# Kernel optimization log

Hardware: AMD Instinct MI355X
Metric: run time of the kernel (lower is better)

## Reference

```python
import jax, jax.numpy as jnp
import numpy as np

N_MID, EMB_DIM, HID, SEQ_LEN, BATCH = 200000, 128, 128, 256, 512


def setup_inputs() -> dict:
    key = jax.random.key(0)
    k1, k2, k3, k4, k5, k6, k7 = jax.random.split(key, 7)
    mid = jax.random.randint(k1, (BATCH,), 0, N_MID, dtype=jnp.int32)
    mid_hist = jax.random.randint(k2, (BATCH, SEQ_LEN), 0, N_MID, dtype=jnp.int32)
    mask = jax.random.randint(k3, (BATCH, SEQ_LEN), 0, 2, dtype=jnp.int32)
    # Embedding table: RandomUniform(-0.05, 0.05) per original init
    emb_table = jax.random.uniform(k4, (N_MID, EMB_DIM), jnp.float32, -0.05, 0.05)
    # Keras GRU (reset_after=True): kernel [D,3H], recurrent_kernel [H,3H], bias [2,3H]
    W = jax.random.normal(k5, (EMB_DIM, 3 * HID), jnp.float32) * 0.05
    U = jax.random.normal(k6, (HID, 3 * HID), jnp.float32) * 0.05
    b = jax.random.normal(k7, (2, 3 * HID), jnp.float32) * 0.05
    return {"mid": mid, "mid_hist": mid_hist, "mask": mask,
            "emb_table": emb_table, "W": W, "U": U, "b": b}


def _masked_gru(hist_emb, mask, W, U, b):
    # hist_emb: [B, T, D], mask: [B, T] int
    B, T, _ = hist_emb.shape
    H = U.shape[0]
    b_in, b_rec = b[0], b[1]
    # precompute input projections once: [B, T, 3H]
    x_proj = jnp.einsum('btd,dh->bth', hist_emb, W) + b_in
    x_proj_t = jnp.swapaxes(x_proj, 0, 1)  # [T, B, 3H]
    mask_t = jnp.swapaxes(mask, 0, 1).astype(bool)  # [T, B]

    def step(h, inp):
        x_t, m_t = inp
        rec = h @ U + b_rec  # [B, 3H]
        xz, xr, xh = x_t[:, :H], x_t[:, H:2 * H], x_t[:, 2 * H:]
        rz, rr, rh = rec[:, :H], rec[:, H:2 * H], rec[:, 2 * H:]
        z = jax.nn.sigmoid(xz + rz)
        r = jax.nn.sigmoid(xr + rr)
        hh = jnp.tanh(xh + r * rh)  # reset_after=True: r applied after recurrent matmul
        h_new = z * h + (1.0 - z) * hh
        h = jnp.where(m_t[:, None], h_new, h)  # masked steps hold state
        return h, None

    h0 = jnp.zeros((B, H), hist_emb.dtype)
    h_final, _ = jax.lax.scan(step, h0, (x_proj_t, mask_t))
    return h_final


def reference(mid, mid_hist, mask, emb_table, W, U, b):
    item_emb = emb_table[mid]            # [B, D]
    hist_emb = emb_table[mid_hist]       # [B, T, D]
    user_vec = _masked_gru(hist_emb, mask, W, U, b)  # [B, H]
    return (user_vec, item_emb)
```

## Files before the change

kernel.cpp:

```cpp
#include <hip/hip_runtime.h>

#define BATCH  512
#define SEQLEN 256
#define EMB    128
#define HID    128
#define LDSROW 136

typedef _Float16 f16;
typedef __attribute__((ext_vector_type(8))) _Float16 half8;
typedef __attribute__((ext_vector_type(4))) _Float16 half4f;
typedef __attribute__((ext_vector_type(4))) float    floatx4;

__device__ __forceinline__ float fast_sigmoid(float x) {
    return __builtin_amdgcn_rcpf(1.0f + __builtin_amdgcn_exp2f(x * -1.4426950408889634f));
}
__device__ __forceinline__ float fast_tanh(float x) {
    float t = __builtin_amdgcn_exp2f(x * 2.8853900817779268f);
    return 1.0f - 2.0f * __builtin_amdgcn_rcpf(t + 1.0f);
}

__global__ void prep_kernel(const int* __restrict__ mask, const int* __restrict__ mid,
                            const float* __restrict__ emb,
                            unsigned* __restrict__ maskP, float* __restrict__ item_out) {
    int tid  = blockIdx.x * blockDim.x + threadIdx.x;
    int nthr = gridDim.x * blockDim.x;
    for (int i = tid; i < 32 * SEQLEN; i += nthr) {
        int blk = i >> 8, t = i & 255;
        unsigned m = 0;
        #pragma unroll
        for (int r = 0; r < 16; ++r)
            m |= (unsigned)(mask[(blk * 16 + r) * SEQLEN + t] & 1) << r;
        maskP[i] = m;
    }
    for (int i = tid; i < BATCH * EMB; i += nthr) {
        int b = i >> 7, d = i & 127;
        item_out[i] = emb[(size_t)mid[b] * EMB + d];
    }
}

__global__ __launch_bounds__(512, 1) void gru_fused(
        const int* __restrict__ mid_hist, const float* __restrict__ emb,
        const float* __restrict__ W, const float* __restrict__ U,
        const float* __restrict__ bvec, const unsigned* __restrict__ maskP,
        float* __restrict__ out_user) {
    __shared__ __align__(16) f16 elds[2][16 * LDSROW];
    __shared__ __align__(16) f16 hpk[16 * LDSROW];

    const int tid   = threadIdx.x;
    const int lane  = tid & 63;
    const int w     = tid >> 6;
    const int l15   = lane & 15;
    const int g4    = lane >> 4;
    const int blk   = blockIdx.x;
    const int bbase = blk * 16;

    half8 uA[3][4], wA[3][4];
    #pragma unroll
    for (int p = 0; p < 3; ++p)
        #pragma unroll
        for (int kt = 0; kt < 4; ++kt) {
            half8 u, v;
            const int j = p * 128 + w * 16 + l15;
            #pragma unroll
            for (int e = 0; e < 8; ++e) {
                int k = kt * 32 + g4 * 8 + e;
                u[e] = (f16)U[k * 384 + j];
                v[e] = (f16)W[k * 384 + j];
            }
            uA[p][kt] = u; wA[p][kt] = v;
        }

    const int jj = w * 16 + g4 * 4;
    float bcz[4], bcr[4], bih[4], brh[4];
    {
        float4 a0 = *(const float4*)(bvec + jj);
        float4 a1 = *(const float4*)(bvec + 384 + jj);
        float4 c0 = *(const float4*)(bvec + 128 + jj);
        float4 c1 = *(const float4*)(bvec + 512 + jj);
        float4 d0 = *(const float4*)(bvec + 256 + jj);
        float4 d1 = *(const float4*)(bvec + 640 + jj);
        bcz[0]=a0.x+a1.x; bcz[1]=a0.y+a1.y; bcz[2]=a0.z+a1.z; bcz[3]=a0.w+a1.w;
        bcr[0]=c0.x+c1.x; bcr[1]=c0.y+c1.y; bcr[2]=c0.z+c1.z; bcr[3]=c0.w+c1.w;
        bih[0]=d0.x; bih[1]=d0.y; bih[2]=d0.z; bih[3]=d0.w;
        brh[0]=d1.x; brh[1]=d1.y; brh[2]=d1.z; brh[3]=d1.w;
    }

    const int r_e = tid >> 5;
    const int c_e = (tid & 31) * 4;

    for (int i = tid; i < 16 * LDSROW; i += 512) hpk[i] = (f16)0.f;

    {
        int i0 = mid_hist[(bbase + r_e) * SEQLEN + 0];
        int i1 = mid_hist[(bbase + r_e) * SEQLEN + 1];
        float4 v0 = *(const float4*)(emb + (size_t)i0 * EMB + c_e);
        float4 v1 = *(const float4*)(emb + (size_t)i1 * EMB + c_e);
        *(half4f*)&elds[0][r_e * LDSROW + c_e] = half4f{(f16)v0.x,(f16)v0.y,(f16)v0.z,(f16)v0.w};
        *(half4f*)&elds[1][r_e * LDSROW + c_e] = half4f{(f16)v1.x,(f16)v1.y,(f16)v1.z,(f16)v1.w};
    }
    __syncthreads();

    int i2 = mid_hist[(bbase + r_e) * SEQLEN + 2];
    int i3 = mid_hist[(bbase + r_e) * SEQLEN + 3];
    float4   eE   = *(const float4*)(emb + (size_t)i2 * EMB + c_e);
    float4   eO   = *(const float4*)(emb + (size_t)i3 * EMB + c_e);
    int      idxE = mid_hist[(bbase + r_e) * SEQLEN + 4];
    int      idxO = mid_hist[(bbase + r_e) * SEQLEN + 5];
    unsigned mskE = maskP[blk * SEQLEN + 0];
    unsigned mskO = maskP[blk * SEQLEN + 1];

    float hreg[4] = {0.f, 0.f, 0.f, 0.f};
    const int aoff  = l15 * LDSROW;
    const int hwoff = l15 * LDSROW + jj;

    auto step = [&](int t, int slot, float4& eBuf, int& idxP, unsigned& mskR) {
        half8 ea[4], ha[4];
        const f16* eb = elds[slot];
        #pragma unroll
        for (int kt = 0; kt < 4; ++kt) {
            ea[kt] = *(const half8*)&eb [aoff + kt * 32 + g4 * 8];
            ha[kt] = *(const half8*)&hpk[aoff + kt * 32 + g4 * 8];
        }
        __builtin_amdgcn_sched_barrier(0);
        asm volatile("s_waitcnt lgkmcnt(0)" ::: "memory");
        __builtin_amdgcn_s_barrier();
        __builtin_amdgcn_sched_barrier(0);

        float4 ev = eBuf;
        *(half4f*)&elds[slot][r_e * LDSROW + c_e] =
            half4f{(f16)ev.x,(f16)ev.y,(f16)ev.z,(f16)ev.w};
        unsigned mval = mskR;
        int ii = idxP;
        eBuf = *(const float4*)(emb + (size_t)ii * EMB + c_e);
        int t6 = t + 6 < SEQLEN ? t + 6 : SEQLEN - 1;
        idxP = mid_hist[(bbase + r_e) * SEQLEN + t6];
        int t2 = t + 2 < SEQLEN ? t + 2 : SEQLEN - 1;
        mskR = maskP[blk * SEQLEN + t2];

        floatx4 az = {0,0,0,0}, ar = {0,0,0,0}, axh = {0,0,0,0}, arh = {0,0,0,0};
        #pragma unroll
        for (int kt = 0; kt < 4; ++kt) {
            az  = __builtin_amdgcn_mfma_f32_16x16x32_f16(wA[0][kt], ea[kt], az,  0,0,0);
            ar  = __builtin_amdgcn_mfma_f32_16x16x32_f16(wA[1][kt], ea[kt], ar,  0,0,0);
            axh = __builtin_amdgcn_mfma_f32_16x16x32_f16(wA[2][kt], ea[kt], axh, 0,0,0);
            az  = __builtin_amdgcn_mfma_f32_16x16x32_f16(uA[0][kt], ha[kt], az,  0,0,0);
            ar  = __builtin_amdgcn_mfma_f32_16x16x32_f16(uA[1][kt], ha[kt], ar,  0,0,0);
            arh = __builtin_amdgcn_mfma_f32_16x16x32_f16(uA[2][kt], ha[kt], arh, 0,0,0);
        }

        const int mbit = (mval >> l15) & 1;
        #pragma unroll
        for (int r = 0; r < 4; ++r) {
            float z  = fast_sigmoid(az[r] + bcz[r]);
            float rg = fast_sigmoid(ar[r] + bcr[r]);
            float hh = fast_tanh(axh[r] + bih[r] + rg * (arh[r] + brh[r]));
            float hn = hh + z * (hreg[r] - hh);
            hreg[r] = mbit ? hn : hreg[r];
        }
        half4f hw = { (f16)hreg[0], (f16)hreg[1], (f16)hreg[2], (f16)hreg[3] };
        *(half4f*)&hpk[hwoff] = hw;
        __builtin_amdgcn_sched_barrier(0);
        asm volatile("s_waitcnt lgkmcnt(0)" ::: "memory");
        __builtin_amdgcn_s_barrier();
        __builtin_amdgcn_sched_barrier(0);
    };

    #pragma unroll 1
    for (int t = 0; t < SEQLEN; t += 2) {
        step(t,     0, eE, idxE, mskE);
        step(t + 1, 1, eO, idxO, mskO);
    }

    float4 o = { hreg[0], hreg[1], hreg[2], hreg[3] };
    *(float4*)(out_user + (size_t)(bbase + l15) * HID + jj) = o;
}

extern "C" void kernel_launch(void* const* d_in, const int* in_sizes, int n_in,
                              void* d_out, int out_size, void* d_ws, size_t ws_size,
                              hipStream_t stream) {
    const int*   mid      = (const int*)d_in[0];
    const int*   mid_hist = (const int*)d_in[1];
    const int*   mask     = (const int*)d_in[2];
    const float* emb      = (const float*)d_in[3];
    const float* W        = (const float*)d_in[4];
    const float* U        = (const float*)d_in[5];
    const float* bvec     = (const float*)d_in[6];

    float* user_out = (float*)d_out;
    float* item_out = (float*)d_out + BATCH * HID;

    unsigned* maskP = (unsigned*)d_ws;

    prep_kernel<<<32, 256, 0, stream>>>(mask, mid, emb, maskP, item_out);
    gru_fused  <<<32, 512, 0, stream>>>(mid_hist, emb, W, U, bvec, maskP, user_out);
}
```

Before: 398.5 us.

## Double-buffer hidden state and 4-slot embedding ring to halve barriers per step

Makes the hidden-state LDS tile double-buffered and the embedding tile a four-slot ring, so each GRU step needs one barrier instead of two. Embedding operands for the next step are prefetched from LDS during the current step. An XOR swizzle replaces the padded row layout to avoid LDS bank conflicts, and the gate math folds the log2e scales into FMAs. The prep kernel is split into mask-packing blocks that stage through LDS and separate item-gather blocks. Risks include ring-slot hazards, a wrong step ordering around the single barrier, and higher register pressure from holding the prefetched operands.

```diff
diff --git a/kernel.cpp b/kernel.cpp
--- a/kernel.cpp
+++ b/kernel.cpp
@@ -4,47 +4,49 @@
 #define SEQLEN 256
 #define EMB    128
 #define HID    128
-#define LDSROW 136
 
 typedef _Float16 f16;
 typedef __attribute__((ext_vector_type(8))) _Float16 half8;
 typedef __attribute__((ext_vector_type(4))) _Float16 half4f;
 typedef __attribute__((ext_vector_type(4))) float    floatx4;
 
-__device__ __forceinline__ float fast_sigmoid(float x) {
-    return __builtin_amdgcn_rcpf(1.0f + __builtin_amdgcn_exp2f(x * -1.4426950408889634f));
-}
-__device__ __forceinline__ float fast_tanh(float x) {
-    float t = __builtin_amdgcn_exp2f(x * 2.8853900817779268f);
-    return 1.0f - 2.0f * __builtin_amdgcn_rcpf(t + 1.0f);
+#define L2E 1.44269504088896340736f
+#define T2E 2.88539008177792681472f
+
+__device__ __forceinline__ int swzB(int byte) {
+    return byte ^ (((byte >> 8) & 7) << 4);
 }
 
 __global__ void prep_kernel(const int* __restrict__ mask, const int* __restrict__ mid,
                             const float* __restrict__ emb,
                             unsigned* __restrict__ maskP, float* __restrict__ item_out) {
-    int tid  = blockIdx.x * blockDim.x + threadIdx.x;
-    int nthr = gridDim.x * blockDim.x;
-    for (int i = tid; i < 32 * SEQLEN; i += nthr) {
-        int blk = i >> 8, t = i & 255;
+    const int bid = blockIdx.x, tid = threadIdx.x;
+    if (bid < 32) {
+        __shared__ int mls[16 * 256];
+        for (int i = tid; i < 16 * 256; i += 256)
+            mls[i] = mask[bid * 16 * 256 + i];
+        __syncthreads();
+        int t = tid;
         unsigned m = 0;
         #pragma unroll
         for (int r = 0; r < 16; ++r)
-            m |= (unsigned)(mask[(blk * 16 + r) * SEQLEN + t] & 1) << r;
-        maskP[i] = m;
-    }
-    for (int i = tid; i < BATCH * EMB; i += nthr) {
-        int b = i >> 7, d = i & 127;
-        item_out[i] = emb[(size_t)mid[b] * EMB + d];
-    }
-}
-
-__global__ __launch_bounds__(512, 1) void gru_fused(
+            m |= (unsigned)(mls[r * 256 + t] & 1) << r;
+        maskP[bid * 256 + t] = m;
+    } else {
+        for (int i = (bid - 32) * 256 + tid; i < BATCH * EMB; i += 224 * 256) {
+            int b = i >> 7, d = i & 127;
+            item_out[i] = emb[(size_t)mid[b] * EMB + d];
+        }
+    }
+}
+
+__global__ __launch_bounds__(512, 2) void gru_fused(
         const int* __restrict__ mid_hist, const float* __restrict__ emb,
         const float* __restrict__ W, const float* __restrict__ U,
         const float* __restrict__ bvec, const unsigned* __restrict__ maskP,
         float* __restrict__ out_user) {
-    __shared__ __align__(16) f16 elds[2][16 * LDSROW];
-    __shared__ __align__(16) f16 hpk[16 * LDSROW];
+    __shared__ __align__(16) f16 hpk[2][16 * 128];
+    __shared__ __align__(16) f16 elds[4][16 * 128];
 
     const int tid   = threadIdx.x;
     const int lane  = tid & 63;
@@ -71,7 +73,7 @@
         }
 
     const int jj = w * 16 + g4 * 4;
-    float bcz[4], bcr[4], bih[4], brh[4];
+    float nbz[4], nbr[4], sxh[4], srh[4];
     {
         float4 a0 = *(const float4*)(bvec + jj);
         float4 a1 = *(const float4*)(bvec + 384 + jj);
@@ -79,63 +81,57 @@
         float4 c1 = *(const float4*)(bvec + 512 + jj);
         float4 d0 = *(const float4*)(bvec + 256 + jj);
         float4 d1 = *(const float4*)(bvec + 640 + jj);
-        bcz[0]=a0.x+a1.x; bcz[1]=a0.y+a1.y; bcz[2]=a0.z+a1.z; bcz[3]=a0.w+a1.w;
-        bcr[0]=c0.x+c1.x; bcr[1]=c0.y+c1.y; bcr[2]=c0.z+c1.z; bcr[3]=c0.w+c1.w;
-        bih[0]=d0.x; bih[1]=d0.y; bih[2]=d0.z; bih[3]=d0.w;
-        brh[0]=d1.x; brh[1]=d1.y; brh[2]=d1.z; brh[3]=d1.w;
-    }
-
-    const int r_e = tid >> 5;
-    const int c_e = (tid & 31) * 4;
-
-    for (int i = tid; i < 16 * LDSROW; i += 512) hpk[i] = (f16)0.f;
+        nbz[0] = -L2E*(a0.x+a1.x); nbz[1] = -L2E*(a0.y+a1.y);
+        nbz[2] = -L2E*(a0.z+a1.z); nbz[3] = -L2E*(a0.w+a1.w);
+        nbr[0] = -L2E*(c0.x+c1.x); nbr[1] = -L2E*(c0.y+c1.y);
+        nbr[2] = -L2E*(c0.z+c1.z); nbr[3] = -L2E*(c0.w+c1.w);
+        sxh[0] =  T2E*d0.x; sxh[1] = T2E*d0.y; sxh[2] = T2E*d0.z; sxh[3] = T2E*d0.w;
+        srh[0] =  T2E*d1.x; srh[1] = T2E*d1.y; srh[2] = T2E*d1.z; srh[3] = T2E*d1.w;
+    }
+
+    int aswz[4];
+    #pragma unroll
+    for (int kt = 0; kt < 4; ++kt)
+        aswz[kt] = swzB(l15 * 256 + kt * 64 + g4 * 16) >> 1;
+    const int hswz = swzB(l15 * 256 + jj * 2) >> 1;
+    const int r_e  = tid >> 5;
+    const int c32  = tid & 31;
+    const int sswz = swzB(r_e * 256 + c32 * 8) >> 1;
+    const int histbase = (bbase + r_e) * SEQLEN;
+    const int mpbase   = blk * SEQLEN;
+
+    for (int i = tid; i < 16 * 128; i += 512) hpk[0][i] = (f16)0.f;
 
     {
-        int i0 = mid_hist[(bbase + r_e) * SEQLEN + 0];
-        int i1 = mid_hist[(bbase + r_e) * SEQLEN + 1];
-        float4 v0 = *(const float4*)(emb + (size_t)i0 * EMB + c_e);
-        float4 v1 = *(const float4*)(emb + (size_t)i1 * EMB + c_e);
-        *(half4f*)&elds[0][r_e * LDSROW + c_e] = half4f{(f16)v0.x,(f16)v0.y,(f16)v0.z,(f16)v0.w};
-        *(half4f*)&elds[1][r_e * LDSROW + c_e] = half4f{(f16)v1.x,(f16)v1.y,(f16)v1.z,(f16)v1.w};
-    }
+        int i0 = mid_hist[histbase + 0];
+        int i1 = mid_hist[histbase + 1];
+        float4 v0 = *(const float4*)(emb + (size_t)i0 * EMB + c32 * 4);
+        float4 v1 = *(const float4*)(emb + (size_t)i1 * EMB + c32 * 4);
+        *(half4f*)&elds[0][sswz] = half4f{(f16)v0.x,(f16)v0.y,(f16)v0.z,(f16)v0.w};
+        *(half4f*)&elds[1][sswz] = half4f{(f16)v1.x,(f16)v1.y,(f16)v1.z,(f16)v1.w};
+    }
+    int i2 = mid_hist[histbase + 2];
+    int i3 = mid_hist[histbase + 3];
+    float4   Ee = *(const float4*)(emb + (size_t)i2 * EMB + c32 * 4);
+    float4   Eo = *(const float4*)(emb + (size_t)i3 * EMB + c32 * 4);
+    int      Ie = mid_hist[histbase + 4];
+    int      Io = mid_hist[histbase + 5];
+    unsigned Me = maskP[mpbase + 0];
+    unsigned Mo = maskP[mpbase + 1];
+
+    float hreg[4] = {0.f, 0.f, 0.f, 0.f};
     __syncthreads();
 
-    int i2 = mid_hist[(bbase + r_e) * SEQLEN + 2];
-    int i3 = mid_hist[(bbase + r_e) * SEQLEN + 3];
-    float4   eE   = *(const float4*)(emb + (size_t)i2 * EMB + c_e);
-    float4   eO   = *(const float4*)(emb + (size_t)i3 * EMB + c_e);
-    int      idxE = mid_hist[(bbase + r_e) * SEQLEN + 4];
-    int      idxO = mid_hist[(bbase + r_e) * SEQLEN + 5];
-    unsigned mskE = maskP[blk * SEQLEN + 0];
-    unsigned mskO = maskP[blk * SEQLEN + 1];
-
-    float hreg[4] = {0.f, 0.f, 0.f, 0.f};
-    const int aoff  = l15 * LDSROW;
-    const int hwoff = l15 * LDSROW + jj;
-
-    auto step = [&](int t, int slot, float4& eBuf, int& idxP, unsigned& mskR) {
-        half8 ea[4], ha[4];
-        const f16* eb = elds[slot];
-        #pragma unroll
-        for (int kt = 0; kt < 4; ++kt) {
-            ea[kt] = *(const half8*)&eb [aoff + kt * 32 + g4 * 8];
-            ha[kt] = *(const half8*)&hpk[aoff + kt * 32 + g4 * 8];
-        }
-        __builtin_amdgcn_sched_barrier(0);
-        asm volatile("s_waitcnt lgkmcnt(0)" ::: "memory");
-        __builtin_amdgcn_s_barrier();
-        __builtin_amdgcn_sched_barrier(0);
-
-        float4 ev = eBuf;
-        *(half4f*)&elds[slot][r_e * LDSROW + c_e] =
-            half4f{(f16)ev.x,(f16)ev.y,(f16)ev.z,(f16)ev.w};
-        unsigned mval = mskR;
-        int ii = idxP;
-        eBuf = *(const float4*)(emb + (size_t)ii * EMB + c_e);
-        int t6 = t + 6 < SEQLEN ? t + 6 : SEQLEN - 1;
-        idxP = mid_hist[(bbase + r_e) * SEQLEN + t6];
-        int t2 = t + 2 < SEQLEN ? t + 2 : SEQLEN - 1;
-        mskR = maskP[blk * SEQLEN + t2];
+    half8 ea[4];
+    #pragma unroll
+    for (int kt = 0; kt < 4; ++kt) ea[kt] = *(const half8*)&elds[0][aswz[kt]];
+
+    auto step = [&](int t, float4& E, int& I, unsigned& M) {
+        const f16* hrd = hpk[t & 1];
+        f16*       hwr = hpk[(t + 1) & 1];
+        half8 ha[4];
+        #pragma unroll
+        for (int kt = 0; kt < 4; ++kt) ha[kt] = *(const half8*)&hrd[aswz[kt]];
 
         floatx4 az = {0,0,0,0}, ar = {0,0,0,0}, axh = {0,0,0,0}, arh = {0,0,0,0};
         #pragma unroll
@@ -143,22 +139,41 @@
             az  = __builtin_amdgcn_mfma_f32_16x16x32_f16(wA[0][kt], ea[kt], az,  0,0,0);
             ar  = __builtin_amdgcn_mfma_f32_16x16x32_f16(wA[1][kt], ea[kt], ar,  0,0,0);
             axh = __builtin_amdgcn_mfma_f32_16x16x32_f16(wA[2][kt], ea[kt], axh, 0,0,0);
+        }
+        #pragma unroll
+        for (int kt = 0; kt < 4; ++kt) {
             az  = __builtin_amdgcn_mfma_f32_16x16x32_f16(uA[0][kt], ha[kt], az,  0,0,0);
             ar  = __builtin_amdgcn_mfma_f32_16x16x32_f16(uA[1][kt], ha[kt], ar,  0,0,0);
             arh = __builtin_amdgcn_mfma_f32_16x16x32_f16(uA[2][kt], ha[kt], arh, 0,0,0);
         }
 
+        *(half4f*)&elds[(t + 2) & 3][sswz] =
+            half4f{(f16)E.x, (f16)E.y, (f16)E.z, (f16)E.w};
+        int ii = I;
+        E = *(const float4*)(emb + (size_t)ii * EMB + c32 * 4);
+        int t6 = t + 6 < SEQLEN ? t + 6 : SEQLEN - 1;
+        I = mid_hist[histbase + t6];
+        unsigned mval = M;
+        M = maskP[mpbase + t + 2];
+        {
+            const f16* erd = elds[(t + 1) & 3];
+            #pragma unroll
+            for (int kt = 0; kt < 4; ++kt) ea[kt] = *(const half8*)&erd[aswz[kt]];
+        }
+
         const int mbit = (mval >> l15) & 1;
         #pragma unroll
         for (int r = 0; r < 4; ++r) {
-            float z  = fast_sigmoid(az[r] + bcz[r]);
-            float rg = fast_sigmoid(ar[r] + bcr[r]);
-            float hh = fast_tanh(axh[r] + bih[r] + rg * (arh[r] + brh[r]));
-            float hn = hh + z * (hreg[r] - hh);
-            hreg[r] = mbit ? hn : hreg[r];
-        }
-        half4f hw = { (f16)hreg[0], (f16)hreg[1], (f16)hreg[2], (f16)hreg[3] };
-        *(half4f*)&hpk[hwoff] = hw;
+            float z  = __builtin_amdgcn_rcpf(1.f + __builtin_amdgcn_exp2f(__builtin_fmaf(az[r], -L2E, nbz[r])));
+            float rg = __builtin_amdgcn_rcpf(1.f + __builtin_amdgcn_exp2f(__builtin_fmaf(ar[r], -L2E, nbr[r])));
+            float u  = __builtin_fmaf(rg, __builtin_fmaf(arh[r], T2E, srh[r]),
+                                          __builtin_fmaf(axh[r], T2E, sxh[r]));
+            float hh = __builtin_fmaf(-2.f, __builtin_amdgcn_rcpf(__builtin_amdgcn_exp2f(u) + 1.f), 1.f);
+            float hn = __builtin_fmaf(z, hreg[r] - hh, hh);
+            hreg[r]  = mbit ? hn : hreg[r];
+        }
+        *(half4f*)&hwr[hswz] = half4f{(f16)hreg[0], (f16)hreg[1], (f16)hreg[2], (f16)hreg[3]};
+
         __builtin_amdgcn_sched_barrier(0);
         asm volatile("s_waitcnt lgkmcnt(0)" ::: "memory");
         __builtin_amdgcn_s_barrier();
@@ -167,8 +182,8 @@
 
     #pragma unroll 1
     for (int t = 0; t < SEQLEN; t += 2) {
-        step(t,     0, eE, idxE, mskE);
-        step(t + 1, 1, eO, idxO, mskO);
+        step(t,     Ee, Ie, Me);
+        step(t + 1, Eo, Io, Mo);
     }
 
     float4 o = { hreg[0], hreg[1], hreg[2], hreg[3] };
@@ -191,6 +206,6 @@
 
     unsigned* maskP = (unsigned*)d_ws;
 
-    prep_kernel<<<32, 256, 0, stream>>>(mask, mid, emb, maskP, item_out);
+    prep_kernel<<<256, 256, 0, stream>>>(mask, mid, emb, maskP, item_out);
     gru_fused  <<<32, 512, 0, stream>>>(mid_hist, emb, W, U, bvec, maskP, user_out);
 }
```

After: 353.1 us. 1.13x faster.
